# Kernel optimization log

Measured on AMD Instinct MI355X. Metric: run time of the kernel, lower is better.

## Reference

```python
import jax, jax.numpy as jnp
import numpy as np

SCALE = 1000.0  # scaling_factor


def setup_inputs() -> dict:
    key = jax.random.key(0)
    ks = jax.random.split(key, 9)
    bs, M, O, J, E = 128, 64, 4096, 64, 256
    return {
        "lbs": jax.random.uniform(ks[0], (bs, O), jnp.float32) * 2000.0,
        "time": jax.random.uniform(ks[1], (bs,), jnp.float32) * 1000.0,
        "is_ready": (jax.random.uniform(ks[2], (bs, O)) < 0.5).astype(jnp.float32),
        "proc_times": jax.random.uniform(ks[3], (bs, M, O), jnp.float32) * 100.0,
        "busy_until": jax.random.uniform(ks[4], (bs, M), jnp.float32) * 2000.0,
        "ma_emb": jax.random.normal(ks[5], (bs, M, E), jnp.float32),
        "W_node": jax.random.normal(ks[6], (2, 3 * E), jnp.float32) * 0.05,
        "W_edge": jax.random.normal(ks[7], (3,), jnp.float32) * 0.5,
        "next_op": jax.random.randint(ks[8], (bs, J), 0, O),
    }


def reference(lbs, time, is_ready, proc_times, busy_until, ma_emb, W_node, W_edge, next_op):
    bs, M, E = ma_emb.shape
    J = next_op.shape[1]
    # node step features: [b, O, 2] gathered to [b, J, 2]
    lbs_n = jnp.clip(lbs - time[:, None], 0.0) / SCALE
    update_feat = jnp.stack((lbs_n, is_ready), axis=-1)                      # [b,O,2]
    job_feat = jnp.take_along_axis(update_feat, next_op[:, :, None], axis=1)  # [b,J,2]
    node_upd = job_feat @ W_node                                             # [b,J,3E]
    # edge step: mask busy machines, gather selected ops, project with 1->3 linear
    ma_busy = busy_until > time[:, None]                                     # [b,M]
    masked = jnp.where(ma_busy[:, :, None], 0.0, proc_times / SCALE)         # [b,M,O]
    job_proc = jnp.take_along_axis(masked, next_op[:, None, :], axis=2)      # [b,M,J]
    job_edge = job_proc.transpose(0, 2, 1)[..., None] * W_edge               # [b,J,M,3]
    edge_upd = jnp.einsum('bjmk,bme->bjke', job_edge, ma_emb).reshape(bs, J, 3 * E)
    updates = node_upd + edge_upd                                            # [b,J,3E]
    return (updates[..., :E], updates[..., E:2 * E], updates[..., 2 * E:])
```

## Files before the change

kernel.cpp:

```cpp
#include <hip/hip_runtime.h>
#include <hip/hip_bf16.h>


#define BS 128
#define MM 64
#define OO 4096
#define JJ 64
#define EE 256
#define JH 8

__global__ __launch_bounds__(256, 4) void jssp_kernel(
    const float* __restrict__ lbs,
    const float* __restrict__ time_,
    const float* __restrict__ isr,
    const float* __restrict__ proc,
    const float* __restrict__ busy,
    const float* __restrict__ emb,
    const float* __restrict__ Wn,
    const float* __restrict__ We,
    const int*   __restrict__ nop,
    float* __restrict__ out)
{
    __shared__ float S[JH][MM];
    __shared__ float aj[JH];
    __shared__ float rj[JH];

    const int hw  = blockIdx.x;
    const int xcd = hw & 7;
    const int k   = hw >> 3;
    const int b   = xcd * 16 + (k >> 3);
    const int jh  = k & 7;

    const int t  = threadIdx.x;
    const float tb = time_[b];


    int   gjj[2], gm[2];
    float gv[2], gbz[2];
    #pragma unroll
    for (int it = 0; it < 2; ++it) {
        const int id = it * 256 + t;
        const int jj = id >> 6;
        const int m  = id & 63;
        const int o  = nop[b * JJ + jh * JH + jj];
        gjj[it] = jj; gm[it] = m;
        gv[it]  = proc[(size_t)(b * MM + m) * OO + (size_t)o];
        gbz[it] = busy[b * MM + m];
    }

    float al = 0.0f, rl = 0.0f;
    if (t < JH) {
        const int o = nop[b * JJ + jh * JH + t];
        al = lbs[b * OO + o];
        rl = isr[b * OO + o];
    }

    float ecol[MM];
    #pragma unroll
    for (int m = 0; m < MM; ++m)
        ecol[m] = emb[(size_t)(b * MM + m) * EE + (size_t)t];

    const float w0a = Wn[t],            w1a = Wn[768 + t];
    const float w0b = Wn[EE + t],       w1b = Wn[768 + EE + t];
    const float w0c = Wn[2 * EE + t],   w1c = Wn[768 + 2 * EE + t];
    const float we0 = We[0], we1 = We[1], we2 = We[2];

    #pragma unroll
    for (int it = 0; it < 2; ++it)
        S[gjj[it]][gm[it]] = (gbz[it] > tb) ? 0.0f : gv[it] * 1e-3f;
    if (t < JH) {
        aj[t] = fmaxf(al - tb, 0.0f) * 1e-3f;
        rj[t] = rl;
    }
    __syncthreads();

    const size_t SZ   = (size_t)BS * JJ * EE;
    const size_t base = (size_t)(b * JJ + jh * JH) * EE + (size_t)t;

    for (int jj = 0; jj < JH; ++jj) {
        const float4* S4 = reinterpret_cast<const float4*>(&S[jj][0]);
        float acc = 0.0f;
        #pragma unroll
        for (int m4 = 0; m4 < MM / 4; ++m4) {
            const float4 s = S4[m4];
            acc = fmaf(s.x, ecol[4 * m4 + 0], acc);
            acc = fmaf(s.y, ecol[4 * m4 + 1], acc);
            acc = fmaf(s.z, ecol[4 * m4 + 2], acc);
            acc = fmaf(s.w, ecol[4 * m4 + 3], acc);
        }
        const float a = aj[jj];
        const float r = rj[jj];
        const size_t off = base + (size_t)jj * EE;
        out[off]          = fmaf(a, w0a, fmaf(r, w1a, we0 * acc));
        out[SZ + off]     = fmaf(a, w0b, fmaf(r, w1b, we1 * acc));
        out[2 * SZ + off] = fmaf(a, w0c, fmaf(r, w1c, we2 * acc));
    }
}

extern "C" void kernel_launch(void* const* d_in, const int* in_sizes, int n_in,
                              void* d_out, int out_size, void* d_ws, size_t ws_size,
                              hipStream_t stream) {
    const float* lbs   = (const float*)d_in[0];
    const float* time_ = (const float*)d_in[1];
    const float* isr   = (const float*)d_in[2];
    const float* proc  = (const float*)d_in[3];
    const float* busy  = (const float*)d_in[4];
    const float* emb   = (const float*)d_in[5];
    const float* Wn    = (const float*)d_in[6];
    const float* We    = (const float*)d_in[7];
    const int*   nop   = (const int*)d_in[8];
    float* out = (float*)d_out;

    jssp_kernel<<<dim3(BS * (JJ / JH)), dim3(256), 0, stream>>>(
        lbs, time_, isr, proc, busy, emb, Wn, We, nop, out);
}
```

Before: 21.86 us.

## Stream embedding columns in chunks with double-buffered registers and higher occupancy

Replaces the 64-register embedding column with two 16-register buffers refilled between compute phases, so global loads of later embedding rows overlap FMAs on earlier ones. Accumulators for all 8 jobs are kept in registers, and launch bounds rise from 4 to 6 blocks per SM to raise occupancy. The proc gather is remapped so consecutive threads vary the job index rather than the machine index, and the shared tile gets padding. Output stores are grouped per projection. The cost is more live accumulators and a tighter register budget, which could cause spills.

```diff
diff --git a/kernel.cpp b/kernel.cpp
--- a/kernel.cpp
+++ b/kernel.cpp
@@ -1,5 +1,4 @@
 #include <hip/hip_runtime.h>
-#include <hip/hip_bf16.h>
 
 
 #define BS 128
@@ -8,8 +7,9 @@
 #define JJ 64
 #define EE 256
 #define JH 8
+#define SP 68
 
-__global__ __launch_bounds__(256, 4) void jssp_kernel(
+__global__ __launch_bounds__(256, 6) void jssp_kernel(
     const float* __restrict__ lbs,
     const float* __restrict__ time_,
     const float* __restrict__ isr,
@@ -21,27 +21,24 @@
     const int*   __restrict__ nop,
     float* __restrict__ out)
 {
-    __shared__ float S[JH][MM];
-    __shared__ float aj[JH];
-    __shared__ float rj[JH];
+    __shared__ float S[JH][SP];
+    __shared__ float aj[JH], rj[JH];
 
     const int hw  = blockIdx.x;
     const int xcd = hw & 7;
     const int k   = hw >> 3;
     const int b   = xcd * 16 + (k >> 3);
     const int jh  = k & 7;
-
-    const int t  = threadIdx.x;
+    const int t   = threadIdx.x;
     const float tb = time_[b];
 
-
+    float gv[2], gbz[2];
     int   gjj[2], gm[2];
-    float gv[2], gbz[2];
     #pragma unroll
     for (int it = 0; it < 2; ++it) {
         const int id = it * 256 + t;
-        const int jj = id >> 6;
-        const int m  = id & 63;
+        const int jj = id & 7;
+        const int m  = id >> 3;
         const int o  = nop[b * JJ + jh * JH + jj];
         gjj[it] = jj; gm[it] = m;
         gv[it]  = proc[(size_t)(b * MM + m) * OO + (size_t)o];
@@ -55,15 +52,17 @@
         rl = isr[b * OO + o];
     }
 
-    float ecol[MM];
-    #pragma unroll
-    for (int m = 0; m < MM; ++m)
-        ecol[m] = emb[(size_t)(b * MM + m) * EE + (size_t)t];
-
     const float w0a = Wn[t],            w1a = Wn[768 + t];
     const float w0b = Wn[EE + t],       w1b = Wn[768 + EE + t];
     const float w0c = Wn[2 * EE + t],   w1c = Wn[768 + 2 * EE + t];
     const float we0 = We[0], we1 = We[1], we2 = We[2];
+
+    const size_t ebase = (size_t)(b * MM) * EE + (size_t)t;
+    float eA[16], eB[16];
+    #pragma unroll
+    for (int i = 0; i < 16; ++i) eA[i] = emb[ebase + (size_t)i * EE];
+    #pragma unroll
+    for (int i = 0; i < 16; ++i) eB[i] = emb[ebase + (size_t)(16 + i) * EE];
 
     #pragma unroll
     for (int it = 0; it < 2; ++it)
@@ -74,27 +73,49 @@
     }
     __syncthreads();
 
+    float acc[JH];
+    #pragma unroll
+    for (int j = 0; j < JH; ++j) acc[j] = 0.0f;
+
+    #define COMP(EREG, C)                                                  \
+        _Pragma("unroll")                                                  \
+        for (int j = 0; j < JH; ++j) {                                     \
+            const float4* S4 = reinterpret_cast<const float4*>(&S[j][(C) * 16]); \
+            _Pragma("unroll")                                              \
+            for (int m4 = 0; m4 < 4; ++m4) {                               \
+                const float4 s = S4[m4];                                   \
+                acc[j] = fmaf(s.x, EREG[4 * m4 + 0], acc[j]);              \
+                acc[j] = fmaf(s.y, EREG[4 * m4 + 1], acc[j]);              \
+                acc[j] = fmaf(s.z, EREG[4 * m4 + 2], acc[j]);              \
+                acc[j] = fmaf(s.w, EREG[4 * m4 + 3], acc[j]);              \
+            }                                                              \
+        }
+
+    COMP(eA, 0);
+    #pragma unroll
+    for (int i = 0; i < 16; ++i) eA[i] = emb[ebase + (size_t)(32 + i) * EE];
+    COMP(eB, 1);
+    #pragma unroll
+    for (int i = 0; i < 16; ++i) eB[i] = emb[ebase + (size_t)(48 + i) * EE];
+    COMP(eA, 2);
+    COMP(eB, 3);
+    #undef COMP
+
     const size_t SZ   = (size_t)BS * JJ * EE;
     const size_t base = (size_t)(b * JJ + jh * JH) * EE + (size_t)t;
 
-    for (int jj = 0; jj < JH; ++jj) {
-        const float4* S4 = reinterpret_cast<const float4*>(&S[jj][0]);
-        float acc = 0.0f;
-        #pragma unroll
-        for (int m4 = 0; m4 < MM / 4; ++m4) {
-            const float4 s = S4[m4];
-            acc = fmaf(s.x, ecol[4 * m4 + 0], acc);
-            acc = fmaf(s.y, ecol[4 * m4 + 1], acc);
-            acc = fmaf(s.z, ecol[4 * m4 + 2], acc);
-            acc = fmaf(s.w, ecol[4 * m4 + 3], acc);
-        }
-        const float a = aj[jj];
-        const float r = rj[jj];
-        const size_t off = base + (size_t)jj * EE;
-        out[off]          = fmaf(a, w0a, fmaf(r, w1a, we0 * acc));
-        out[SZ + off]     = fmaf(a, w0b, fmaf(r, w1b, we1 * acc));
-        out[2 * SZ + off] = fmaf(a, w0c, fmaf(r, w1c, we2 * acc));
-    }
+    #pragma unroll
+    for (int j = 0; j < JH; ++j)
+        out[base + (size_t)j * EE] =
+            fmaf(aj[j], w0a, fmaf(rj[j], w1a, we0 * acc[j]));
+    #pragma unroll
+    for (int j = 0; j < JH; ++j)
+        out[SZ + base + (size_t)j * EE] =
+            fmaf(aj[j], w0b, fmaf(rj[j], w1b, we1 * acc[j]));
+    #pragma unroll
+    for (int j = 0; j < JH; ++j)
+        out[2 * SZ + base + (size_t)j * EE] =
+            fmaf(aj[j], w0c, fmaf(rj[j], w1c, we2 * acc[j]));
 }
 
 extern "C" void kernel_launch(void* const* d_in, const int* in_sizes, int n_in,
```

Result: faster. 21.20 us (median of 2 runs) (-3.0%).

## Retile per-thread work to 4 embedding columns by 2 jobs with float4 I/O

Applied to the files above, without the earlier changes.

Each thread now computes a 2-job by 4-column register tile instead of one column across all 8 jobs. This replaces the 64-register embedding column with double-buffered float4 loads streamed through the m loop. The proc gather is reordered so that consecutive threads write to different S rows, and S is padded to 68 floats per row to avoid LDS bank conflicts. Outputs and weights move to float4 vector accesses, which cuts register pressure and instruction count but adds wider scattered loads.

```diff
diff --git a/kernel.cpp b/kernel.cpp
--- a/kernel.cpp
+++ b/kernel.cpp
@@ -1,5 +1,4 @@
 #include <hip/hip_runtime.h>
-#include <hip/hip_bf16.h>
 
 
 #define BS 128
@@ -8,6 +7,7 @@
 #define JJ 64
 #define EE 256
 #define JH 8
+#define SP 68
 
 __global__ __launch_bounds__(256, 4) void jssp_kernel(
     const float* __restrict__ lbs,
@@ -21,27 +21,26 @@
     const int*   __restrict__ nop,
     float* __restrict__ out)
 {
-    __shared__ float S[JH][MM];
-    __shared__ float aj[JH];
-    __shared__ float rj[JH];
+    __shared__ float S[JH][SP];
+    __shared__ float aj[JH], rj[JH];
 
     const int hw  = blockIdx.x;
     const int xcd = hw & 7;
     const int k   = hw >> 3;
     const int b   = xcd * 16 + (k >> 3);
     const int jh  = k & 7;
-
-    const int t  = threadIdx.x;
+    const int t   = threadIdx.x;
+    const int el  = t & 63;
+    const int jl  = t >> 6;
     const float tb = time_[b];
 
-
+    float gv[2], gbz[2];
     int   gjj[2], gm[2];
-    float gv[2], gbz[2];
     #pragma unroll
     for (int it = 0; it < 2; ++it) {
         const int id = it * 256 + t;
-        const int jj = id >> 6;
-        const int m  = id & 63;
+        const int jj = id & 7;
+        const int m  = id >> 3;
         const int o  = nop[b * JJ + jh * JH + jj];
         gjj[it] = jj; gm[it] = m;
         gv[it]  = proc[(size_t)(b * MM + m) * OO + (size_t)o];
@@ -55,15 +54,12 @@
         rl = isr[b * OO + o];
     }
 
-    float ecol[MM];
-    #pragma unroll
-    for (int m = 0; m < MM; ++m)
-        ecol[m] = emb[(size_t)(b * MM + m) * EE + (size_t)t];
-
-    const float w0a = Wn[t],            w1a = Wn[768 + t];
-    const float w0b = Wn[EE + t],       w1b = Wn[768 + EE + t];
-    const float w0c = Wn[2 * EE + t],   w1c = Wn[768 + 2 * EE + t];
-    const float we0 = We[0], we1 = We[1], we2 = We[2];
+    const float* embB = emb + (size_t)(b * MM) * EE + (size_t)(el * 4);
+    float4 ea0 = *(const float4*)(embB + 0 * EE);
+    float4 ea1 = *(const float4*)(embB + 1 * EE);
+    float4 ea2 = *(const float4*)(embB + 2 * EE);
+    float4 ea3 = *(const float4*)(embB + 3 * EE);
+    float4 eb0, eb1, eb2, eb3;
 
     #pragma unroll
     for (int it = 0; it < 2; ++it)
@@ -74,27 +70,80 @@
     }
     __syncthreads();
 
+    const int j0 = jl * 2;
+    const float4* S4A = reinterpret_cast<const float4*>(&S[j0][0]);
+    const float4* S4B = reinterpret_cast<const float4*>(&S[j0 + 1][0]);
+
+    float4 accA; accA.x = accA.y = accA.z = accA.w = 0.0f;
+    float4 accB; accB.x = accB.y = accB.z = accB.w = 0.0f;
+
+#define FMA4(ACC, SS, EV)                         \
+    ACC.x = fmaf(SS, EV.x, ACC.x);                \
+    ACC.y = fmaf(SS, EV.y, ACC.y);                \
+    ACC.z = fmaf(SS, EV.z, ACC.z);                \
+    ACC.w = fmaf(SS, EV.w, ACC.w);
+
+#define CHUNK(SA, SB, E0, E1, E2, E3)             \
+    FMA4(accA, SA.x, E0) FMA4(accA, SA.y, E1)     \
+    FMA4(accA, SA.z, E2) FMA4(accA, SA.w, E3)     \
+    FMA4(accB, SB.x, E0) FMA4(accB, SB.y, E1)     \
+    FMA4(accB, SB.z, E2) FMA4(accB, SB.w, E3)
+
+    #pragma unroll
+    for (int cc = 0; cc < 8; ++cc) {
+        const int c0 = 2 * cc, c1 = 2 * cc + 1;
+        eb0 = *(const float4*)(embB + (size_t)(c1 * 4 + 0) * EE);
+        eb1 = *(const float4*)(embB + (size_t)(c1 * 4 + 1) * EE);
+        eb2 = *(const float4*)(embB + (size_t)(c1 * 4 + 2) * EE);
+        eb3 = *(const float4*)(embB + (size_t)(c1 * 4 + 3) * EE);
+        {
+            const float4 sA = S4A[c0], sB = S4B[c0];
+            CHUNK(sA, sB, ea0, ea1, ea2, ea3)
+        }
+        if (cc < 7) {
+            const int cn = 2 * cc + 2;
+            ea0 = *(const float4*)(embB + (size_t)(cn * 4 + 0) * EE);
+            ea1 = *(const float4*)(embB + (size_t)(cn * 4 + 1) * EE);
+            ea2 = *(const float4*)(embB + (size_t)(cn * 4 + 2) * EE);
+            ea3 = *(const float4*)(embB + (size_t)(cn * 4 + 3) * EE);
+        }
+        {
+            const float4 sA = S4A[c1], sB = S4B[c1];
+            CHUNK(sA, sB, eb0, eb1, eb2, eb3)
+        }
+    }
+#undef CHUNK
+#undef FMA4
+
+    const float a0 = aj[j0],     r0 = rj[j0];
+    const float a1 = aj[j0 + 1], r1 = rj[j0 + 1];
+    const float we0 = We[0], we1 = We[1], we2 = We[2];
+    const float4 w0a = *(const float4*)(Wn + el * 4);
+    const float4 w1a = *(const float4*)(Wn + 768 + el * 4);
+    const float4 w0b = *(const float4*)(Wn + 256 + el * 4);
+    const float4 w1b = *(const float4*)(Wn + 1024 + el * 4);
+    const float4 w0c = *(const float4*)(Wn + 512 + el * 4);
+    const float4 w1c = *(const float4*)(Wn + 1280 + el * 4);
+
+    auto epi = [](float A, float R, const float4& ACC, const float4& W0,
+                  const float4& W1, float WE) {
+        float4 v;
+        v.x = fmaf(A, W0.x, fmaf(R, W1.x, WE * ACC.x));
+        v.y = fmaf(A, W0.y, fmaf(R, W1.y, WE * ACC.y));
+        v.z = fmaf(A, W0.z, fmaf(R, W1.z, WE * ACC.z));
+        v.w = fmaf(A, W0.w, fmaf(R, W1.w, WE * ACC.w));
+        return v;
+    };
+
     const size_t SZ   = (size_t)BS * JJ * EE;
-    const size_t base = (size_t)(b * JJ + jh * JH) * EE + (size_t)t;
+    const size_t base = (size_t)(b * JJ + jh * JH) * EE + (size_t)(el * 4);
 
-    for (int jj = 0; jj < JH; ++jj) {
-        const float4* S4 = reinterpret_cast<const float4*>(&S[jj][0]);
-        float acc = 0.0f;
-        #pragma unroll
-        for (int m4 = 0; m4 < MM / 4; ++m4) {
-            const float4 s = S4[m4];
-            acc = fmaf(s.x, ecol[4 * m4 + 0], acc);
-            acc = fmaf(s.y, ecol[4 * m4 + 1], acc);
-            acc = fmaf(s.z, ecol[4 * m4 + 2], acc);
-            acc = fmaf(s.w, ecol[4 * m4 + 3], acc);
-        }
-        const float a = aj[jj];
-        const float r = rj[jj];
-        const size_t off = base + (size_t)jj * EE;
-        out[off]          = fmaf(a, w0a, fmaf(r, w1a, we0 * acc));
-        out[SZ + off]     = fmaf(a, w0b, fmaf(r, w1b, we1 * acc));
-        out[2 * SZ + off] = fmaf(a, w0c, fmaf(r, w1c, we2 * acc));
-    }
+    *(float4*)(out + base + (size_t)j0 * EE)             = epi(a0, r0, accA, w0a, w1a, we0);
+    *(float4*)(out + base + (size_t)(j0 + 1) * EE)       = epi(a1, r1, accB, w0a, w1a, we0);
+    *(float4*)(out + SZ + base + (size_t)j0 * EE)        = epi(a0, r0, accA, w0b, w1b, we1);
+    *(float4*)(out + SZ + base + (size_t)(j0 + 1) * EE)  = epi(a1, r1, accB, w0b, w1b, we1);
+    *(float4*)(out + 2 * SZ + base + (size_t)j0 * EE)    = epi(a0, r0, accA, w0c, w1c, we2);
+    *(float4*)(out + 2 * SZ + base + (size_t)(j0 + 1) * EE) = epi(a1, r1, accB, w0c, w1c, we2);
 }
 
 extern "C" void kernel_launch(void* const* d_in, const int* in_sizes, int n_in,
```

New measurement: 23.92 us. +9.4%, slower.
